# Performance work log

Hardware: AMD Instinct MI355X
Metric: run time of the kernel (lower is better)

## Reference

```python
import jax, jax.numpy as jnp
import numpy as np

EPS = 1e-6  # torch F.pairwise_distance default eps added to the difference


def _gather(src, idx):
    # src: [S, B, D], idx: [B, K] -> out[b, k] = src[idx[b, k], b], shape [B, K, D]
    B, K = idx.shape
    out = src[idx, jnp.arange(B)[:, None]]
    return out.reshape(B * K, src.shape[-1])


def _pairwise_l2(a, b):
    d = a - b + EPS
    return jnp.sqrt(jnp.sum(d * d, axis=-1))


def setup_inputs() -> dict:
    key = jax.random.key(0)
    ks = jax.random.split(key, 8)
    S, B, K, D = 2048, 256, 11, 128
    return {
        "anchor_near_tensor": jax.random.normal(ks[0], (S, B, D), dtype=jnp.float32),
        "anchor_far_tensor": jax.random.normal(ks[1], (S, B, D), dtype=jnp.float32),
        "near_anchor_indexs": jax.random.randint(ks[2], (B, K), 0, S),
        "far_anchor_indexs": jax.random.randint(ks[3], (B, K), 0, S),
        "near_indexs": jax.random.randint(ks[4], (B, K), 0, S),
        "far_indexs": jax.random.randint(ks[5], (B, K), 0, S),
        "near_target": jax.random.uniform(ks[6], (B * K,), dtype=jnp.float32),
        "far_target": jax.random.uniform(ks[7], (B * K,), dtype=jnp.float32),
    }


def reference(anchor_near_tensor, anchor_far_tensor, near_anchor_indexs,
              far_anchor_indexs, near_indexs, far_indexs, near_target, far_target):
    na = _gather(anchor_near_tensor, near_anchor_indexs)  # [B*K, D]
    fa = _gather(anchor_far_tensor, far_anchor_indexs)
    ne = _gather(anchor_near_tensor, near_indexs)
    fe = _gather(anchor_far_tensor, far_indexs)
    near_predict = jnp.exp(-_pairwise_l2(na, ne))
    far_predict = jnp.exp(-_pairwise_l2(fa, fe))
    near_loss = near_predict - near_target
    far_loss = far_predict - far_target
    return jnp.sum(near_loss * near_loss) + jnp.sum(far_loss * far_loss)
```

## Files before the change

### kernel.cpp

```cpp
#include <hip/hip_runtime.h>

#define EPS 1e-6f

__global__ __launch_bounds__(256) void traj_loss_partial_kernel(
    const float* __restrict__ anear,
    const float* __restrict__ afar,
    const int* __restrict__ na_idx,
    const int* __restrict__ fa_idx,
    const int* __restrict__ ne_idx,
    const int* __restrict__ fe_idx,
    const float* __restrict__ ntgt,
    const float* __restrict__ ftgt,
    float* __restrict__ partials,
    int B, int K)
{
    const int gtid = blockIdx.x * blockDim.x + threadIdx.x;
    const int wave = gtid >> 6;
    const int lane = threadIdx.x & 63;
    const int wid  = threadIdx.x >> 6;
    const int BK = B * K;
    const int total = 2 * BK;

    __shared__ float warp_part[4];

    float loss2 = 0.0f;
    if (wave < total) {
        const int side = (wave >= BK) ? 1 : 0;
        const int row  = side ? (wave - BK) : wave;
        const int b    = row / K;

        const float* src = side ? afar   : anear;
        const int*   ia  = side ? fa_idx : na_idx;
        const int*   ib  = side ? fe_idx : ne_idx;
        const float* tg  = side ? ftgt   : ntgt;

        const int sa = ia[row];
        const int sb = ib[row];

        const float2* pa = (const float2*)(src + ((size_t)sa * B + b) * 128);
        const float2* pb = (const float2*)(src + ((size_t)sb * B + b) * 128);

        const float2 va = pa[lane];
        const float2 vb = pb[lane];
        const float dx = va.x - vb.x + EPS;
        const float dy = va.y - vb.y + EPS;
        float s = dx * dx + dy * dy;

        #pragma unroll
        for (int off = 32; off > 0; off >>= 1)
            s += __shfl_down(s, off, 64);

        if (lane == 0) {
            const float pred = __expf(-sqrtf(s));
            const float l = pred - tg[row];
            loss2 = l * l;
        }
    }

    if (lane == 0) warp_part[wid] = loss2;
    __syncthreads();
    if (threadIdx.x == 0) {
        partials[blockIdx.x] = warp_part[0] + warp_part[1] + warp_part[2] + warp_part[3];
    }
}

__global__ __launch_bounds__(256) void reduce_partials_kernel(
    const float* __restrict__ partials, float* __restrict__ out, int n)
{
    float s = 0.0f;
    for (int i = threadIdx.x; i < n; i += 256)
        s += partials[i];

    #pragma unroll
    for (int off = 32; off > 0; off >>= 1)
        s += __shfl_down(s, off, 64);

    __shared__ float warp_part[4];
    const int lane = threadIdx.x & 63;
    const int wid  = threadIdx.x >> 6;
    if (lane == 0) warp_part[wid] = s;
    __syncthreads();
    if (threadIdx.x == 0)
        out[0] = warp_part[0] + warp_part[1] + warp_part[2] + warp_part[3];
}

extern "C" void kernel_launch(void* const* d_in, const int* in_sizes, int n_in,
                              void* d_out, int out_size, void* d_ws, size_t ws_size,
                              hipStream_t stream) {
    const float* anear = (const float*)d_in[0];
    const float* afar  = (const float*)d_in[1];
    const int* na_idx  = (const int*)d_in[2];
    const int* fa_idx  = (const int*)d_in[3];
    const int* ne_idx  = (const int*)d_in[4];
    const int* fe_idx  = (const int*)d_in[5];
    const float* ntgt  = (const float*)d_in[6];
    const float* ftgt  = (const float*)d_in[7];
    float* out = (float*)d_out;
    float* partials = (float*)d_ws;

    const int B = 256;
    const int K = 11;

    const int totalWaves = 2 * B * K;
    const int wavesPerBlock = 4;
    const int grid = (totalWaves + wavesPerBlock - 1) / wavesPerBlock;

    traj_loss_partial_kernel<<<grid, 256, 0, stream>>>(anear, afar, na_idx, fa_idx,
                                                       ne_idx, fe_idx, ntgt, ftgt,
                                                       partials, B, K);
    reduce_partials_kernel<<<1, 256, 0, stream>>>(partials, out, grid);
}
```

Before: 12.25 us.

## Process near and far pairs in one wave with larger blocks

Each wave now computes both the near and far distance for a row, issuing four gathered loads at once instead of two. Blocks grow to 1024 threads, so the grid shrinks to 176 blocks, and the final reduction drops its loop because the partial count fits in one block. This aims to raise loads in flight per wave and cut block count. The trade-off is that fewer blocks than CUs may leave hardware idle, and the loop-free reduction silently drops partials if the grid ever exceeds 256.

```diff
diff --git a/kernel.cpp b/kernel.cpp
--- a/kernel.cpp
+++ b/kernel.cpp
@@ -2,7 +2,7 @@
 
 #define EPS 1e-6f
 
-__global__ __launch_bounds__(256) void traj_loss_partial_kernel(
+__global__ __launch_bounds__(1024) void traj_loss_partial_kernel(
     const float* __restrict__ anear,
     const float* __restrict__ afar,
     const int* __restrict__ na_idx,
@@ -14,74 +14,79 @@
     float* __restrict__ partials,
     int B, int K)
 {
-    const int gtid = blockIdx.x * blockDim.x + threadIdx.x;
-    const int wave = gtid >> 6;
-    const int lane = threadIdx.x & 63;
-    const int wid  = threadIdx.x >> 6;
-    const int BK = B * K;
-    const int total = 2 * BK;
-
-    __shared__ float warp_part[4];
+    const int wave_g = (blockIdx.x * 1024 + threadIdx.x) >> 6;
+    const int lane   = threadIdx.x & 63;
+    const int wid    = threadIdx.x >> 6;
+    const int BK     = B * K;
 
     float loss2 = 0.0f;
-    if (wave < total) {
-        const int side = (wave >= BK) ? 1 : 0;
-        const int row  = side ? (wave - BK) : wave;
-        const int b    = row / K;
+    if (wave_g < BK) {
+        const int row = wave_g;
+        const int b   = row / K;
 
-        const float* src = side ? afar   : anear;
-        const int*   ia  = side ? fa_idx : na_idx;
-        const int*   ib  = side ? fe_idx : ne_idx;
-        const float* tg  = side ? ftgt   : ntgt;
+        const int sa = na_idx[row];
+        const int sb = ne_idx[row];
+        const int sc = fa_idx[row];
+        const int sd = fe_idx[row];
 
-        const int sa = ia[row];
-        const int sb = ib[row];
-
-        const float2* pa = (const float2*)(src + ((size_t)sa * B + b) * 128);
-        const float2* pb = (const float2*)(src + ((size_t)sb * B + b) * 128);
+        const float2* pa = (const float2*)(anear + ((size_t)sa * B + b) * 128);
+        const float2* pb = (const float2*)(anear + ((size_t)sb * B + b) * 128);
+        const float2* pc = (const float2*)(afar  + ((size_t)sc * B + b) * 128);
+        const float2* pd = (const float2*)(afar  + ((size_t)sd * B + b) * 128);
 
         const float2 va = pa[lane];
         const float2 vb = pb[lane];
+        const float2 vc = pc[lane];
+        const float2 vd = pd[lane];
+
         const float dx = va.x - vb.x + EPS;
         const float dy = va.y - vb.y + EPS;
-        float s = dx * dx + dy * dy;
+        float s1 = dx * dx + dy * dy;
+
+        const float ex = vc.x - vd.x + EPS;
+        const float ey = vc.y - vd.y + EPS;
+        float s2 = ex * ex + ey * ey;
 
         #pragma unroll
-        for (int off = 32; off > 0; off >>= 1)
-            s += __shfl_down(s, off, 64);
+        for (int off = 32; off > 0; off >>= 1) {
+            s1 += __shfl_down(s1, off, 64);
+            s2 += __shfl_down(s2, off, 64);
+        }
 
         if (lane == 0) {
-            const float pred = __expf(-sqrtf(s));
-            const float l = pred - tg[row];
-            loss2 = l * l;
+            const float l1 = __expf(-sqrtf(s1)) - ntgt[row];
+            const float l2 = __expf(-sqrtf(s2)) - ftgt[row];
+            loss2 = l1 * l1 + l2 * l2;
         }
     }
 
-    if (lane == 0) warp_part[wid] = loss2;
+    __shared__ float wp[16];
+    if (lane == 0) wp[wid] = loss2;
     __syncthreads();
     if (threadIdx.x == 0) {
-        partials[blockIdx.x] = warp_part[0] + warp_part[1] + warp_part[2] + warp_part[3];
+        float s = 0.0f;
+        #pragma unroll
+        for (int i = 0; i < 16; ++i) s += wp[i];
+        partials[blockIdx.x] = s;
     }
 }
 
 __global__ __launch_bounds__(256) void reduce_partials_kernel(
     const float* __restrict__ partials, float* __restrict__ out, int n)
 {
-    float s = 0.0f;
-    for (int i = threadIdx.x; i < n; i += 256)
-        s += partials[i];
+    float s = (threadIdx.x < n) ? partials[threadIdx.x] : 0.0f;
 
     #pragma unroll
     for (int off = 32; off > 0; off >>= 1)
         s += __shfl_down(s, off, 64);
 
-    __shared__ float warp_part[4];
+    __shared__ float wp[4];
     const int lane = threadIdx.x & 63;
     const int wid  = threadIdx.x >> 6;
-    if (lane == 0) warp_part[wid] = s;
+    if (lane == 0) wp[wid] = s;
     __syncthreads();
     if (threadIdx.x == 0)
-        out[0] = warp_part[0] + warp_part[1] + warp_part[2] + warp_part[3];
+        out[0] = wp[0] + wp[1] + wp[2] + wp[3];
 }
 
 extern "C" void kernel_launch(void* const* d_in, const int* in_sizes, int n_in,
@@ -100,13 +105,12 @@
 
     const int B = 256;
     const int K = 11;
+    const int BK = B * K;
+    const int wavesPerBlock = 16;
+    const int grid = (BK + wavesPerBlock - 1) / wavesPerBlock;
 
-    const int totalWaves = 2 * B * K;
-    const int wavesPerBlock = 4;
-    const int grid = (totalWaves + wavesPerBlock - 1) / wavesPerBlock;
-
-    traj_loss_partial_kernel<<<grid, 256, 0, stream>>>(anear, afar, na_idx, fa_idx,
-                                                       ne_idx, fe_idx, ntgt, ftgt,
-                                                       partials, B, K);
+    traj_loss_partial_kernel<<<grid, 1024, 0, stream>>>(anear, afar, na_idx, fa_idx,
+                                                        ne_idx, fe_idx, ntgt, ftgt,
+                                                        partials, B, K);
     reduce_partials_kernel<<<1, 256, 0, stream>>>(partials, out, grid);
 }
```

New measurement: 18.36 us. 49.8% more time.
